# Kernel optimization log

Measured on AMD Instinct MI355X. Metric: run time of the kernel, lower is better.

Reference implementation:

```python
import jax, jax.numpy as jnp
import numpy as np

N = 100000      # number of nodes
D = 64          # node_dim
H = 128         # hidden
E = 1600000     # number of undirected edges (each yields 2 directed messages)


def setup_inputs() -> dict:
    key = jax.random.key(0)
    k_nodes, k_edges, k_w1, k_w2 = jax.random.split(key, 4)
    nodes = jax.random.normal(k_nodes, (N, D), dtype=jnp.float32)
    edges = jax.random.randint(k_edges, (E, 2), 0, N, dtype=jnp.int32)
    # msg = Linear(2D, H) -> ReLU -> Linear(H, D); Kaiming-ish init
    W1 = jax.random.normal(k_w1, (2 * D, H), dtype=jnp.float32) * (1.0 / np.sqrt(2 * D))
    b1 = jnp.zeros((H,), dtype=jnp.float32)
    W2 = jax.random.normal(k_w2, (H, D), dtype=jnp.float32) * (1.0 / np.sqrt(H))
    b2 = jnp.zeros((D,), dtype=jnp.float32)
    return {"nodes": nodes, "edges": edges, "W1": W1, "b1": b1, "W2": W2, "b2": b2}


def reference(nodes, edges, W1, b1, W2, b2):
    # nodes: [N, D]; edges: [E, 2] int32
    i = edges[:, 0]
    j = edges[:, 1]
    h_i = nodes[i]            # [E, D] gather
    h_j = nodes[j]            # [E, D] gather

    def mlp(x):               # [E, 2D] -> [E, D]
        return jax.nn.relu(x @ W1 + b1) @ W2 + b2

    m_ij = mlp(jnp.concatenate([h_i, h_j], axis=-1))  # message to node i
    m_ji = mlp(jnp.concatenate([h_j, h_i], axis=-1))  # message to node j

    # out = nodes.clone(); out[i] += m_ij; out[j] += m_ji  (all from ORIGINAL nodes)
    out = nodes \
        + jax.ops.segment_sum(m_ij, i, num_segments=N) \
        + jax.ops.segment_sum(m_ji, j, num_segments=N)
    return out
```

## Files before the change

kernel.cpp:

```cpp
#include <hip/hip_runtime.h>

#define DFEAT 64
#define NEDGES 1600000

typedef __bf16 bf16x8 __attribute__((ext_vector_type(8)));
typedef float f32x4 __attribute__((ext_vector_type(4)));

__device__ __forceinline__ __bf16 f2bf(float f) {
  unsigned u = __builtin_bit_cast(unsigned, f);
  u += 0x7FFFu + ((u >> 16) & 1u);
  unsigned short s = (unsigned short)(u >> 16);
  return __builtin_bit_cast(__bf16, s);
}

__global__ void init_out(const float* __restrict__ nodes, float* __restrict__ out) {
  int i = blockIdx.x * blockDim.x + threadIdx.x;
  ((float4*)out)[i] = ((const float4*)nodes)[i];
}

__launch_bounds__(256, 2)
__global__ void edge_mlp(const float* __restrict__ nodes,
                         const int* __restrict__ edges,
                         const float* __restrict__ W1,
                         const float* __restrict__ b1,
                         const float* __restrict__ W2,
                         const float* __restrict__ b2,
                         float* __restrict__ out) {
  __shared__ __bf16 w1t[128 * 128];
  __shared__ __bf16 w2t[64 * 128];
  __shared__ __bf16 hid[4][16 * 128];

  const int tid = threadIdx.x;

  for (int it = 0; it < 16; ++it) {
    int q = it * 256 + tid;
    int k = q >> 5;
    int nc = (q & 31) << 2;
    float4 v = ((const float4*)W1)[q];
    float vv[4] = {v.x, v.y, v.z, v.w};
#pragma unroll
    for (int c = 0; c < 4; ++c) {
      int n = nc + c;
      int blk = (k >> 3) ^ (n & 15);
      w1t[n * 128 + blk * 8 + (k & 7)] = f2bf(vv[c]);
    }
  }
  for (int it = 0; it < 8; ++it) {
    int q = it * 256 + tid;
    int k = q >> 4;
    int nc = (q & 15) << 2;
    float4 v = ((const float4*)W2)[q];
    float vv[4] = {v.x, v.y, v.z, v.w};
#pragma unroll
    for (int c = 0; c < 4; ++c) {
      int n = nc + c;
      int blk = (k >> 3) ^ (n & 15);
      w2t[n * 128 + blk * 8 + (k & 7)] = f2bf(vv[c]);
    }
  }
  __syncthreads();

  const int lane = tid & 63;
  const int wave = tid >> 6;
  const int col = lane & 15;
  const int quad = lane >> 4;
  __bf16* myhid = hid[wave];

  float b1v[8], b2v[4];
#pragma unroll
  for (int nt = 0; nt < 8; ++nt) b1v[nt] = b1[nt * 16 + col];
#pragma unroll
  for (int nt = 0; nt < 4; ++nt) b2v[nt] = b2[nt * 16 + col];

  for (int t = 0; t < 8; ++t) {
    const int e0 = blockIdx.x * 512 + wave * 128 + t * 16;
    const int e = e0 + col;
    const int ie = edges[2 * e];
    const int je = edges[2 * e + 1];

    bf16x8 af[4];
#pragma unroll
    for (int kt = 0; kt < 4; ++kt) {
      int k = kt * 32 + quad * 8;
      const float* src = (k < 64) ? (nodes + (long)ie * 64 + k)
                                  : (nodes + (long)je * 64 + (k - 64));
      float4 v0 = ((const float4*)src)[0];
      float4 v1 = ((const float4*)src)[1];
      bf16x8 a;
      a[0] = f2bf(v0.x); a[1] = f2bf(v0.y); a[2] = f2bf(v0.z); a[3] = f2bf(v0.w);
      a[4] = f2bf(v1.x); a[5] = f2bf(v1.y); a[6] = f2bf(v1.z); a[7] = f2bf(v1.w);
      af[kt] = a;
    }

#pragma unroll
    for (int dir = 0; dir < 2; ++dir) {
      f32x4 acc[8];
#pragma unroll
      for (int nt = 0; nt < 8; ++nt) acc[nt] = (f32x4)0.0f;
#pragma unroll
      for (int kt = 0; kt < 4; ++kt) {
        int kblk = kt * 4 + quad;
        if (dir) kblk ^= 8;
#pragma unroll
        for (int nt = 0; nt < 8; ++nt) {
          int n = nt * 16 + col;
          const bf16x8 bf = *(const bf16x8*)&w1t[n * 128 + ((kblk ^ (n & 15)) << 3)];
          acc[nt] = __builtin_amdgcn_mfma_f32_16x16x32_bf16(af[kt], bf, acc[nt], 0, 0, 0);
        }
      }
#pragma unroll
      for (int nt = 0; nt < 8; ++nt) {
        int unit = nt * 16 + col;
#pragma unroll
        for (int r = 0; r < 4; ++r) {
          int m = quad * 4 + r;
          float h = acc[nt][r] + b1v[nt];
          h = h > 0.0f ? h : 0.0f;
          myhid[m * 128 + (((unit >> 3) ^ m) << 3) + (unit & 7)] = f2bf(h);
        }
      }

      f32x4 acc2[4];
#pragma unroll
      for (int nt = 0; nt < 4; ++nt) acc2[nt] = (f32x4)0.0f;
#pragma unroll
      for (int kt = 0; kt < 4; ++kt) {
        int kblk = kt * 4 + quad;
        const bf16x8 ah = *(const bf16x8*)&myhid[col * 128 + ((kblk ^ col) << 3)];
#pragma unroll
        for (int nt = 0; nt < 4; ++nt) {
          int n = nt * 16 + col;
          const bf16x8 bf = *(const bf16x8*)&w2t[n * 128 + ((kblk ^ (n & 15)) << 3)];
          acc2[nt] = __builtin_amdgcn_mfma_f32_16x16x32_bf16(ah, bf, acc2[nt], 0, 0, 0);
        }
      }

#pragma unroll
      for (int r = 0; r < 4; ++r) {
        int em = quad * 4 + r;
        int node = __shfl(dir == 0 ? ie : je, em, 64);
        float* dst = out + (long)node * 64;
#pragma unroll
        for (int nt = 0; nt < 4; ++nt) {
          atomicAdd(dst + nt * 16 + col, acc2[nt][r] + b2v[nt]);
        }
      }
    }
  }
}

extern "C" void kernel_launch(void* const* d_in, const int* in_sizes, int n_in,
                              void* d_out, int out_size, void* d_ws, size_t ws_size,
                              hipStream_t stream) {
  const float* nodes = (const float*)d_in[0];
  const int*   edges = (const int*)d_in[1];
  const float* W1    = (const float*)d_in[2];
  const float* b1    = (const float*)d_in[3];
  const float* W2    = (const float*)d_in[4];
  const float* b2    = (const float*)d_in[5];
  float* out = (float*)d_out;

  init_out<<<6250, 256, 0, stream>>>(nodes, out);
  edge_mlp<<<3125, 256, 0, stream>>>(nodes, edges, W1, b1, W2, b2, out);
}
```

Measured before the change: 772.4 us.

## Replace atomic edge scatter with CSR-grouped per-node message aggregation

Builds a CSR adjacency on the device each call (histogram, single-block scan, atomic scatter of neighbour ids), then gives each destination node one wave that walks its neighbours and sums messages in registers. The destination-node half of the first layer is computed once per node and reused for all its edges, and the b2 bias is folded in as degree times b2. This removes the per-element float atomics into the output and the redundant first-layer work, and writes each output row once. In exchange it adds several preprocessing kernels, a serial single-block scan, a workspace requirement with a fallback to the old path, and load imbalance from uneven node degrees.

Measured after the change: 1.031 ms. +33.5%, slower.

```diff
diff --git a/kernel.cpp b/kernel.cpp
--- a/kernel.cpp
+++ b/kernel.cpp
@@ -2,9 +2,11 @@
 
 #define DFEAT 64
 #define NEDGES 1600000
+#define NNODES 100000
 
 typedef __bf16 bf16x8 __attribute__((ext_vector_type(8)));
 typedef float f32x4 __attribute__((ext_vector_type(4)));
+typedef unsigned short u16x8 __attribute__((ext_vector_type(8)));
 
 __device__ __forceinline__ __bf16 f2bf(float f) {
   unsigned u = __builtin_bit_cast(unsigned, f);
@@ -12,6 +14,224 @@
   unsigned short s = (unsigned short)(u >> 16);
   return __builtin_bit_cast(__bf16, s);
 }
+
+
+__global__ void prep_k(const float* __restrict__ nodes,
+                       const float* __restrict__ W1,
+                       const float* __restrict__ W2,
+                       unsigned* __restrict__ cnt,
+                       __bf16* __restrict__ wimg,
+                       __bf16* __restrict__ nbf) {
+  int t = blockIdx.x * 256 + threadIdx.x;
+  {
+    float4 v0 = ((const float4*)nodes)[t * 2];
+    float4 v1 = ((const float4*)nodes)[t * 2 + 1];
+    bf16x8 o;
+    o[0] = f2bf(v0.x); o[1] = f2bf(v0.y); o[2] = f2bf(v0.z); o[3] = f2bf(v0.w);
+    o[4] = f2bf(v1.x); o[5] = f2bf(v1.y); o[6] = f2bf(v1.z); o[7] = f2bf(v1.w);
+    ((bf16x8*)nbf)[t] = o;
+  }
+  if (t < NNODES) cnt[t] = 0u;
+  if (t < 16384) {
+    int k = t >> 7, n = t & 127;
+    wimg[n * 128 + (((k >> 3) ^ (n & 15)) << 3) + (k & 7)] = f2bf(W1[t]);
+  } else if (t < 24576) {
+    int u = t - 16384;
+    int k = u >> 6, n = u & 63;
+    wimg[16384 + n * 128 + (((k >> 3) ^ (n & 15)) << 3) + (k & 7)] = f2bf(W2[u]);
+  }
+}
+
+__global__ void hist_k(const int* __restrict__ edges, unsigned* __restrict__ cnt) {
+  int t = blockIdx.x * 256 + threadIdx.x;
+  int2 e = ((const int2*)edges)[t];
+  atomicAdd(&cnt[e.x], 1u);
+  atomicAdd(&cnt[e.y], 1u);
+}
+
+__global__ void scan_k(const unsigned* __restrict__ cnt,
+                       unsigned* __restrict__ off,
+                       unsigned* __restrict__ cur) {
+  __shared__ unsigned s[1024];
+  const int tid = threadIdx.x;
+  const int CH = 98;
+  int b0 = tid * CH;
+  int b1 = b0 + CH; if (b1 > NNODES) b1 = NNODES;
+  unsigned loc = 0;
+  for (int i = b0; i < b1; ++i) loc += cnt[i];
+  s[tid] = loc;
+  __syncthreads();
+  for (int d = 1; d < 1024; d <<= 1) {
+    unsigned tv = (tid >= d) ? s[tid - d] : 0u;
+    __syncthreads();
+    s[tid] += tv;
+    __syncthreads();
+  }
+  unsigned run = (tid > 0) ? s[tid - 1] : 0u;
+  for (int i = b0; i < b1; ++i) {
+    off[i] = run; cur[i] = run; run += cnt[i];
+  }
+  if (tid == 1023) off[NNODES] = s[1023];
+}
+
+__global__ void scat_k(const int* __restrict__ edges,
+                       unsigned* __restrict__ cur,
+                       unsigned* __restrict__ rec) {
+  int t = blockIdx.x * 256 + threadIdx.x;
+  int2 e = ((const int2*)edges)[t];
+  unsigned p = atomicAdd(&cur[e.x], 1u);
+  rec[p] = (unsigned)e.y;
+  unsigned q = atomicAdd(&cur[e.y], 1u);
+  rec[q] = (unsigned)e.x;
+}
+
+__launch_bounds__(256, 2)
+__global__ void gnn_k(const __bf16* __restrict__ nbf,
+                      const float* __restrict__ nodes,
+                      const unsigned* __restrict__ off,
+                      const unsigned* __restrict__ rec,
+                      const __bf16* __restrict__ wimg,
+                      const float* __restrict__ b1,
+                      const float* __restrict__ b2,
+                      float* __restrict__ out) {
+  __shared__ __align__(16) __bf16 w1t[128 * 128];
+  __shared__ __align__(16) __bf16 w2t[64 * 128];
+  __shared__ __align__(16) __bf16 hid[4][16 * 128];
+
+  const int tid = threadIdx.x;
+
+  {
+    const u16x8* s1 = (const u16x8*)wimg;
+    u16x8* d1 = (u16x8*)w1t;
+#pragma unroll
+    for (int it = 0; it < 8; ++it) d1[it * 256 + tid] = s1[it * 256 + tid];
+    const u16x8* s2 = (const u16x8*)(wimg + 16384);
+    u16x8* d2 = (u16x8*)w2t;
+#pragma unroll
+    for (int it = 0; it < 4; ++it) d2[it * 256 + tid] = s2[it * 256 + tid];
+  }
+  __syncthreads();
+
+  const int lane = tid & 63, wave = tid >> 6;
+  const int col = lane & 15, quad = lane >> 4;
+  __bf16* myhid = hid[wave];
+
+  const int bid = blockIdx.x;
+  const int wg = (bid & 7) * 3125 + (bid >> 3);
+  const int v = wg * 4 + wave;
+
+  float b1v[8];
+#pragma unroll
+  for (int nt = 0; nt < 8; ++nt) b1v[nt] = b1[nt * 16 + col];
+  const float b2l = b2[lane];
+
+  const unsigned beg = off[v], end = off[v + 1];
+  const int deg = (int)(end - beg);
+  const int ntile = (deg + 15) >> 4;
+
+  const bf16x8* nrow = (const bf16x8*)(nbf + (long)v * 64);
+  const bf16x8 af0 = nrow[quad];
+  const bf16x8 af1 = nrow[4 + quad];
+  f32x4 accv[8];
+#pragma unroll
+  for (int nt = 0; nt < 8; ++nt) accv[nt] = (f32x4)0.0f;
+#pragma unroll
+  for (int kt = 0; kt < 2; ++kt) {
+    const int kblk = kt * 4 + quad;
+    const bf16x8 a = kt ? af1 : af0;
+#pragma unroll
+    for (int nt = 0; nt < 8; ++nt) {
+      const int n = nt * 16 + col;
+      const bf16x8 bf = *(const bf16x8*)&w1t[n * 128 + ((kblk ^ (n & 15)) << 3)];
+      accv[nt] = __builtin_amdgcn_mfma_f32_16x16x32_bf16(a, bf, accv[nt], 0, 0, 0);
+    }
+  }
+
+  float part[4] = {0.f, 0.f, 0.f, 0.f};
+
+  bf16x8 a2, a3;
+  {
+    int other0 = v;
+    if (ntile) {
+      unsigned rr = beg + (unsigned)col;
+      if (rr < end) other0 = (int)rec[rr];
+    }
+    const bf16x8* orow = (const bf16x8*)(nbf + (long)other0 * 64);
+    a2 = orow[quad]; a3 = orow[4 + quad];
+  }
+
+  for (int t = 0; t < ntile; ++t) {
+    const unsigned base = beg + (unsigned)(t * 16);
+
+    int othern = v;
+    {
+      unsigned rrn = base + 16u + (unsigned)col;
+      if (rrn < end) othern = (int)rec[rrn];
+    }
+    const bf16x8* prow = (const bf16x8*)(nbf + (long)othern * 64);
+    const bf16x8 n2 = prow[quad];
+    const bf16x8 n3 = prow[4 + quad];
+
+    f32x4 acc[8];
+#pragma unroll
+    for (int nt = 0; nt < 8; ++nt) {
+      const int n = nt * 16 + col;
+      const bf16x8 bf2 = *(const bf16x8*)&w1t[n * 128 + (((8 + quad) ^ (n & 15)) << 3)];
+      const bf16x8 bf3 = *(const bf16x8*)&w1t[n * 128 + (((12 + quad) ^ (n & 15)) << 3)];
+      f32x4 tmp = __builtin_amdgcn_mfma_f32_16x16x32_bf16(a2, bf2, accv[nt], 0, 0, 0);
+      acc[nt] = __builtin_amdgcn_mfma_f32_16x16x32_bf16(a3, bf3, tmp, 0, 0, 0);
+    }
+
+#pragma unroll
+    for (int nt = 0; nt < 8; ++nt) {
+      const int unit = nt * 16 + col;
+#pragma unroll
+      for (int r = 0; r < 4; ++r) {
+        const int m = quad * 4 + r;
+        float h = acc[nt][r] + b1v[nt];
+        h = h > 0.0f ? h : 0.0f;
+        myhid[m * 128 + (((unit >> 3) ^ m) << 3) + (unit & 7)] = f2bf(h);
+      }
+    }
+
+    f32x4 acc2[4];
+#pragma unroll
+    for (int nt = 0; nt < 4; ++nt) acc2[nt] = (f32x4)0.0f;
+#pragma unroll
+    for (int kt = 0; kt < 4; ++kt) {
+      const int kblk = kt * 4 + quad;
+      const bf16x8 ah = *(const bf16x8*)&myhid[col * 128 + ((kblk ^ col) << 3)];
+#pragma unroll
+      for (int nt = 0; nt < 4; ++nt) {
+        const int n = nt * 16 + col;
+        const bf16x8 bf = *(const bf16x8*)&w2t[n * 128 + ((kblk ^ (n & 15)) << 3)];
+        acc2[nt] = __builtin_amdgcn_mfma_f32_16x16x32_bf16(ah, bf, acc2[nt], 0, 0, 0);
+      }
+    }
+
+#pragma unroll
+    for (int r = 0; r < 4; ++r) {
+      const bool valid = (base + (unsigned)(quad * 4 + r)) < end;
+#pragma unroll
+      for (int nt = 0; nt < 4; ++nt) part[nt] += valid ? acc2[nt][r] : 0.0f;
+    }
+
+    a2 = n2; a3 = n3;
+  }
+
+#pragma unroll
+  for (int nt = 0; nt < 4; ++nt) {
+    part[nt] += __shfl_xor(part[nt], 16, 64);
+    part[nt] += __shfl_xor(part[nt], 32, 64);
+  }
+  const float v01 = (quad & 1) ? part[1] : part[0];
+  const float v23 = (quad & 1) ? part[3] : part[2];
+  const float val = (quad & 2) ? v23 : v01;
+
+  const long o = (long)v * 64 + lane;
+  out[o] = nodes[o] + val + (float)deg * b2l;
+}
+
 
 __global__ void init_out(const float* __restrict__ nodes, float* __restrict__ out) {
   int i = blockIdx.x * blockDim.x + threadIdx.x;
@@ -149,6 +369,7 @@
   }
 }
 
+
 extern "C" void kernel_launch(void* const* d_in, const int* in_sizes, int n_in,
                               void* d_out, int out_size, void* d_ws, size_t ws_size,
                               hipStream_t stream) {
@@ -160,6 +381,26 @@
   const float* b2    = (const float*)d_in[5];
   float* out = (float*)d_out;
 
-  init_out<<<6250, 256, 0, stream>>>(nodes, out);
-  edge_mlp<<<3125, 256, 0, stream>>>(nodes, edges, W1, b1, W2, b2, out);
-}
+  char* w = (char*)d_ws;
+  auto al = [](size_t x) { return (x + 255) & ~(size_t)255; };
+  size_t o = 0;
+  unsigned* cnt = (unsigned*)(w + o); o = al(o + (size_t)NNODES * 4);
+  unsigned* off = (unsigned*)(w + o); o = al(o + ((size_t)NNODES + 1) * 4);
+  unsigned* cur = (unsigned*)(w + o); o = al(o + (size_t)NNODES * 4);
+  unsigned* rec = (unsigned*)(w + o); o = al(o + (size_t)2 * NEDGES * 4);
+  __bf16* wimg  = (__bf16*)(w + o);   o = al(o + (size_t)24576 * 2);
+  __bf16* nbf   = (__bf16*)(w + o);   o = al(o + (size_t)NNODES * 64 * 2);
+  const size_t need = o;
+
+  if (d_ws == nullptr || ws_size < need) {
+    init_out<<<6250, 256, 0, stream>>>(nodes, out);
+    edge_mlp<<<3125, 256, 0, stream>>>(nodes, edges, W1, b1, W2, b2, out);
+    return;
+  }
+
+  prep_k<<<3125, 256, 0, stream>>>(nodes, W1, W2, cnt, wimg, nbf);
+  hist_k<<<6250, 256, 0, stream>>>(edges, cnt);
+  scan_k<<<1, 1024, 0, stream>>>(cnt, off, cur);
+  scat_k<<<6250, 256, 0, stream>>>(edges, cur, rec);
+  gnn_k<<<25000, 256, 0, stream>>>(nbf, nodes, off, rec, wimg, b1, b2, out);
+}
```
